# Kernel optimization log

Measured on AMD Instinct MI355X. Metric: run time of the kernel, lower is better.

Reference implementation:

```python
import jax, jax.numpy as jnp
import numpy as np

POOLER_SIZE = 56
SPATIAL_SCALE = 0.25
B, P, K, H, W, A = 4, 512, 4, 200, 336, 14
IMG_H, IMG_W = H / SPATIAL_SCALE, W / SPATIAL_SCALE


def _roi_align_one(feat, boxes):
    """torchvision RoIAlign (aligned=False, sampling_ratio=1).
    feat: [K, H, W]; boxes: [P, 4] as (x1, y1, x2, y2) in image coords.
    Returns [P, K, ps, ps]."""
    Kc, Hf, Wf = feat.shape
    ps = POOLER_SIZE
    s = SPATIAL_SCALE
    x1 = boxes[:, 0] * s
    y1 = boxes[:, 1] * s
    x2 = boxes[:, 2] * s
    y2 = boxes[:, 3] * s
    rw = jnp.maximum(x2 - x1, 1.0)  # non-aligned mode clamps roi size to >= 1
    rh = jnp.maximum(y2 - y1, 1.0)
    bw = rw / ps
    bh = rh / ps
    grid = jnp.arange(ps, dtype=feat.dtype) + 0.5  # sampling_ratio=1 -> bin center
    xs = x1[:, None] + grid[None, :] * bw[:, None]  # [P, ps]
    ys = y1[:, None] + grid[None, :] * bh[:, None]  # [P, ps]
    xx = jnp.broadcast_to(xs[:, None, :], (xs.shape[0], ps, ps))  # [P, ps, ps]
    yy = jnp.broadcast_to(ys[:, :, None], (ys.shape[0], ps, ps))
    valid = (yy > -1.0) & (yy < Hf) & (xx > -1.0) & (xx < Wf)
    y = jnp.clip(yy, 0.0, Hf - 1)
    x = jnp.clip(xx, 0.0, Wf - 1)
    y0 = jnp.floor(y).astype(jnp.int32)
    x0 = jnp.floor(x).astype(jnp.int32)
    y1i = jnp.minimum(y0 + 1, Hf - 1)
    x1i = jnp.minimum(x0 + 1, Wf - 1)
    ly = y - y0
    lx = x - x0
    f = feat.reshape(Kc, Hf * Wf)

    def gather(yi, xi):
        idx = (yi * Wf + xi).reshape(-1)
        return jnp.take(f, idx, axis=1).reshape((Kc,) + yi.shape)  # [K, P, ps, ps]

    w00 = ((1.0 - ly) * (1.0 - lx))[None]
    w01 = ((1.0 - ly) * lx)[None]
    w10 = (ly * (1.0 - lx))[None]
    w11 = (ly * lx)[None]
    v = (gather(y0, x0) * w00 + gather(y0, x1i) * w01 +
         gather(y1i, x0) * w10 + gather(y1i, x1i) * w11)
    v = v * valid[None].astype(feat.dtype)
    return jnp.transpose(v, (1, 0, 2, 3))  # [P, K, ps, ps]


def _bilinear_resize_ac(x, ps):
    """F.interpolate(mode='bilinear', align_corners=True) on last two dims (square a->ps)."""
    a = x.shape[-1]
    src = jnp.arange(ps, dtype=x.dtype) * ((a - 1) / (ps - 1))
    i0 = jnp.clip(jnp.floor(src).astype(jnp.int32), 0, a - 2)
    i1 = i0 + 1
    t = src - i0.astype(x.dtype)
    rows = x[..., i0, :] * (1.0 - t)[:, None] + x[..., i1, :] * t[:, None]  # [..., ps, a]
    out = rows[..., :, i0] * (1.0 - t) + rows[..., :, i1] * t  # [..., ps, ps]
    return out


def setup_inputs() -> dict:
    key = jax.random.key(0)
    k1, k2, k3, k4, k5, k6 = jax.random.split(key, 6)
    bases = jax.random.normal(k1, (B, K, H, W), dtype=jnp.float32)
    attention_proposals = jax.random.normal(k2, (B, P, K, A, A), dtype=jnp.float32)
    # realistic boxes inside an 800x1344 image
    x1 = jax.random.uniform(k3, (B, P)) * (IMG_W - 64.0)
    y1 = jax.random.uniform(k4, (B, P)) * (IMG_H - 64.0)
    bw = 32.0 + jax.random.uniform(k5, (B, P)) * 256.0
    bh = 32.0 + jax.random.uniform(k6, (B, P)) * 256.0
    x2 = jnp.minimum(x1 + bw, IMG_W)
    y2 = jnp.minimum(y1 + bh, IMG_H)
    box_proposals = jnp.stack([x1, y1, x2, y2], axis=-1).astype(jnp.float32)  # [B, P, 4]
    return {"bases": bases, "box_proposals": box_proposals,
            "attention_proposals": attention_proposals}


def reference(bases, box_proposals, attention_proposals):
    ps = POOLER_SIZE
    rois = jax.vmap(_roi_align_one)(bases, box_proposals)  # [B, P, K, ps, ps]
    attn = _bilinear_resize_ac(attention_proposals, ps)    # [B, P, K, ps, ps]
    attn = jax.nn.softmax(attn, axis=2)                    # softmax over num_bases
    return (attn * rois).sum(axis=2)                       # [B, P, ps, ps]
```

## Files before the change

kernel.cpp:

```cpp
#include <hip/hip_runtime.h>
#include <math.h>

#define B_  4
#define P_  512
#define K_  4
#define H_  200
#define W_  336
#define A_  14
#define PS_ 56
#define SCALE_ 0.25f
#define HW_    (H_ * W_)
#define PLB_   (HW_ * 16)
#define ROWB_  (W_ * 16)
#define RROWB_ (PS_ * K_ * 4)

#if __has_builtin(__builtin_amdgcn_exp2f)
#define EXP2F(x) __builtin_amdgcn_exp2f(x)
#else
#define EXP2F(x) exp2f(x)
#endif

static __device__ __forceinline__ unsigned f2bf(float x) {
    unsigned u = __float_as_uint(x);
    return (u + 0x7fffu + ((u >> 16) & 1u)) >> 16;
}
static __device__ __forceinline__ unsigned pk2(float a, float b) {
    return f2bf(a) | (f2bf(b) << 16);
}
#define LOF(u) __uint_as_float((u) << 16)
#define HIF(u) __uint_as_float((u) & 0xffff0000u)

__global__ __launch_bounds__(256) void transpose_bases(
    const float* __restrict__ bases, uint4* __restrict__ ws)
{
    const int i = blockIdx.x * 256 + threadIdx.x;
    if (i >= B_ * HW_) return;
    const int b = i / HW_;
    const int r = i - b * HW_;
    const int x = r % W_;
    const int dn = (x < W_ - 1) ? 1 : 0;
    const float* src = bases + (size_t)b * (K_ * HW_) + r;
    const float v0 = src[0 * HW_],      v1 = src[1 * HW_];
    const float v2 = src[2 * HW_],      v3 = src[3 * HW_];
    const float n0 = src[0 * HW_ + dn], n1 = src[1 * HW_ + dn];
    const float n2 = src[2 * HW_ + dn], n3 = src[3 * HW_ + dn];
    uint4 w;
    w.x = pk2(v0, v1); w.y = pk2(v2, v3);
    w.z = pk2(n0, n1); w.w = pk2(n2, n3);
    ws[i] = w;
}

__global__ __launch_bounds__(448) void blender_kernel(
    const uint4* __restrict__ wsb,
    const float* __restrict__ boxes,
    const float* __restrict__ attn,
    float* __restrict__ out)
{
    const int tid = threadIdx.x;
    const int bp  = blockIdx.x;
    const int b   = bp >> 9;

    __shared__ float  smTile[K_ * A_ * A_];
    __shared__ float  smR[A_ * PS_ * K_];
    __shared__ float4 smX[PS_];
    __shared__ float4 smY[PS_];
    __shared__ float2 smAY[PS_];

    const float* ap = attn + (size_t)bp * (K_ * A_ * A_);
    for (int i = tid; i < K_ * A_ * A_; i += 448)
        smTile[i] = __builtin_nontemporal_load(ap + i);

    const float* bx = boxes + (size_t)bp * 4;
    const float rr = 13.0f / 55.0f;

    if (tid < PS_) {
        const int px = tid;
        const float x1 = bx[0] * SCALE_;
        const float x2 = bx[2] * SCALE_;
        const float bw = fmaxf(x2 - x1, 1.0f) * (1.0f / PS_);
        const float sx = x1 + (px + 0.5f) * bw;
        const float vx = (sx > -1.0f && sx < (float)W_) ? 1.0f : 0.0f;
        const float cx = fminf(fmaxf(sx, 0.0f), (float)(W_ - 1));
        const int   x0 = (int)cx;
        const float lx = cx - (float)x0;
        float4 v;
        v.x = __int_as_float(x0 * 16);
        v.y = (1.0f - lx) * vx;
        v.z = lx * vx;
        v.w = 0.0f;
        smX[px] = v;
    } else if (tid >= 64 && tid < 64 + PS_) {
        const int py = tid - 64;
        const float y1 = bx[1] * SCALE_;
        const float y2 = bx[3] * SCALE_;
        const float bh = fmaxf(y2 - y1, 1.0f) * (1.0f / PS_);
        const float sy = y1 + (py + 0.5f) * bh;
        const float vy = (sy > -1.0f && sy < (float)H_) ? 1.0f : 0.0f;
        const float cy = fminf(fmaxf(sy, 0.0f), (float)(H_ - 1));
        const int   y0 = (int)cy;
        const int   y1i = min(y0 + 1, H_ - 1);
        const float ly = cy - (float)y0;
        float4 v;
        v.x = __int_as_float(y0 * ROWB_);
        v.y = __int_as_float((y1i - y0) * ROWB_);
        v.z = (1.0f - ly) * vy;
        v.w = ly * vy;
        smY[py] = v;
        const float srcy = (float)py * rr;
        const int iy0 = min((int)srcy, A_ - 2);
        float2 a;
        a.x = __int_as_float(iy0 * RROWB_);
        a.y = srcy - (float)iy0;
        smAY[py] = a;
    }
    __syncthreads();

    const float LOG2E = 1.4426950408889634f;
    for (int i = tid; i < K_ * A_ * PS_; i += 448) {
        const int k  = i / (A_ * PS_);
        const int r1 = i - k * (A_ * PS_);
        const int ay = r1 / PS_;
        const int px = r1 - ay * PS_;
        const float srcx = (float)px * rr;
        const int ix0 = min((int)srcx, A_ - 2);
        const float tx = srcx - (float)ix0;
        const float* t = smTile + k * (A_ * A_) + ay * A_ + ix0;
        smR[(ay * PS_ + px) * K_ + k] = (t[0] + tx * (t[1] - t[0])) * LOG2E;
    }
    __syncthreads();

    const char* fb = (const char*)wsb + (size_t)b * PLB_;
    float* outp = out + (size_t)bp * (PS_ * PS_);

    const int px  = tid % PS_;
    const int py0 = tid / PS_;

    const float4 X = smX[px];
    const unsigned xb = (unsigned)__float_as_int(X.x);
    const float wl = X.y, wh = X.z;
    const char* smRbase = (const char*)smR + (px << 4);

    struct PState {
        uint4 r0, r1;
        float wy0, wy1, ty;
        int   ayo;
    };

    auto issue = [&](int t, PState& S) {
        const int py = py0 + 8 * t;
        const float4 Y  = smY[py];
        const float2 AY = smAY[py];
        const unsigned o0 = (unsigned)__float_as_int(Y.x) + xb;
        const unsigned o1 = o0 + (unsigned)__float_as_int(Y.y);
        S.r0 = *(const uint4*)(fb + o0);
        S.r1 = *(const uint4*)(fb + o1);
        S.wy0 = Y.z; S.wy1 = Y.w;
        S.ty = AY.y; S.ayo = __float_as_int(AY.x);
    };

    auto compute = [&](const PState& S) -> float {
        const float wy0 = S.wy0, wy1 = S.wy1, ty = S.ty;
        const float r0a = fmaf(LOF(S.r0.z), wh, LOF(S.r0.x) * wl);
        const float r0b = fmaf(HIF(S.r0.z), wh, HIF(S.r0.x) * wl);
        const float r0c = fmaf(LOF(S.r0.w), wh, LOF(S.r0.y) * wl);
        const float r0d = fmaf(HIF(S.r0.w), wh, HIF(S.r0.y) * wl);
        const float r1a = fmaf(LOF(S.r1.z), wh, LOF(S.r1.x) * wl);
        const float r1b = fmaf(HIF(S.r1.z), wh, HIF(S.r1.x) * wl);
        const float r1c = fmaf(LOF(S.r1.w), wh, LOF(S.r1.y) * wl);
        const float r1d = fmaf(HIF(S.r1.w), wh, HIF(S.r1.y) * wl);
        const float v0 = fmaf(r1a, wy1, r0a * wy0);
        const float v1 = fmaf(r1b, wy1, r0b * wy0);
        const float v2 = fmaf(r1c, wy1, r0c * wy0);
        const float v3 = fmaf(r1d, wy1, r0d * wy0);

        const float4 a0v = *(const float4*)(smRbase + S.ayo);
        const float4 a1v = *(const float4*)(smRbase + S.ayo + RROWB_);
        const float e0 = EXP2F(fmaf(ty, a1v.x - a0v.x, a0v.x));
        const float e1 = EXP2F(fmaf(ty, a1v.y - a0v.y, a0v.y));
        const float e2 = EXP2F(fmaf(ty, a1v.z - a0v.z, a0v.z));
        const float e3 = EXP2F(fmaf(ty, a1v.w - a0v.w, a0v.w));

        const float s = (e0 + e1) + (e2 + e3);
        float acc = e0 * v0;
        acc = fmaf(e1, v1, acc);
        acc = fmaf(e2, v2, acc);
        acc = fmaf(e3, v3, acc);
        return acc * __builtin_amdgcn_rcpf(s);
    };

    PState SA, SB;
    issue(0, SA);
    #pragma unroll
    for (int g = 0; g < 6; g += 2) {
        issue(g + 1, SB);
        __builtin_nontemporal_store(compute(SA), outp + tid + 448 * g);
        issue(g + 2, SA);
        __builtin_nontemporal_store(compute(SB), outp + tid + 448 * (g + 1));
    }
    __builtin_nontemporal_store(compute(SA), outp + tid + 448 * 6);
}

extern "C" void kernel_launch(void* const* d_in, const int* in_sizes, int n_in,
                              void* d_out, int out_size, void* d_ws, size_t ws_size,
                              hipStream_t stream) {
    const float* bases = (const float*)d_in[0];
    const float* boxes = (const float*)d_in[1];
    const float* attn  = (const float*)d_in[2];
    float* out = (float*)d_out;
    uint4* wsb = (uint4*)d_ws;

    transpose_bases<<<dim3((B_ * HW_ + 255) / 256), dim3(256), 0, stream>>>(bases, wsb);
    blender_kernel<<<dim3(B_ * P_), dim3(448), 0, stream>>>(wsb, boxes, attn, out);
}
```

Measured before the change: 90.29 us.

## Halve packed bases workspace and process two ROIs per block

The transpose kernel now packs only the 4 bf16 channels of each pixel into 8 bytes, instead of also storing a copy of the right neighbour. The gather reads 16 unaligned bytes to pick up both the pixel and its right neighbour. This halves workspace writes and the cache footprint. The blender kernel also handles two ROIs per 448-thread block with a reworked pipelined loop, halving block count and spreading setup over more work. Risks: unaligned 16-byte loads may split into two accesses, the final pixel read runs 8 bytes past the workspace end, and fewer blocks may lower occupancy.

```diff
diff --git a/kernel.cpp b/kernel.cpp
--- a/kernel.cpp
+++ b/kernel.cpp
@@ -10,8 +10,8 @@
 #define PS_ 56
 #define SCALE_ 0.25f
 #define HW_    (H_ * W_)
-#define PLB_   (HW_ * 16)
-#define ROWB_  (W_ * 16)
+#define ROWB_  (W_ * 8)
+#define PLB_   (HW_ * 8)
 #define RROWB_ (PS_ * K_ * 4)
 
 #if __has_builtin(__builtin_amdgcn_exp2f)
@@ -30,51 +30,53 @@
 #define LOF(u) __uint_as_float((u) << 16)
 #define HIF(u) __uint_as_float((u) & 0xffff0000u)
 
+static __device__ __forceinline__ uint4 ld16u8(const char* p) {
+    uint4 q;
+    __builtin_memcpy(&q, (const char*)__builtin_assume_aligned(p, 8), 16);
+    return q;
+}
+
 __global__ __launch_bounds__(256) void transpose_bases(
-    const float* __restrict__ bases, uint4* __restrict__ ws)
+    const float* __restrict__ bases, unsigned long long* __restrict__ ws)
 {
     const int i = blockIdx.x * 256 + threadIdx.x;
     if (i >= B_ * HW_) return;
     const int b = i / HW_;
     const int r = i - b * HW_;
-    const int x = r % W_;
-    const int dn = (x < W_ - 1) ? 1 : 0;
     const float* src = bases + (size_t)b * (K_ * HW_) + r;
-    const float v0 = src[0 * HW_],      v1 = src[1 * HW_];
-    const float v2 = src[2 * HW_],      v3 = src[3 * HW_];
-    const float n0 = src[0 * HW_ + dn], n1 = src[1 * HW_ + dn];
-    const float n2 = src[2 * HW_ + dn], n3 = src[3 * HW_ + dn];
-    uint4 w;
-    w.x = pk2(v0, v1); w.y = pk2(v2, v3);
-    w.z = pk2(n0, n1); w.w = pk2(n2, n3);
-    ws[i] = w;
+    const unsigned lo = pk2(src[0 * HW_], src[1 * HW_]);
+    const unsigned hi = pk2(src[2 * HW_], src[3 * HW_]);
+    const unsigned long long w = (unsigned long long)lo
+                               | ((unsigned long long)hi << 32);
+    __builtin_nontemporal_store(w, ws + i);
 }
 
 __global__ __launch_bounds__(448) void blender_kernel(
-    const uint4* __restrict__ wsb,
+    const unsigned long long* __restrict__ wsb,
     const float* __restrict__ boxes,
     const float* __restrict__ attn,
     float* __restrict__ out)
 {
     const int tid = threadIdx.x;
-    const int bp  = blockIdx.x;
-    const int b   = bp >> 9;
-
-    __shared__ float  smTile[K_ * A_ * A_];
-    __shared__ float  smR[A_ * PS_ * K_];
-    __shared__ float4 smX[PS_];
-    __shared__ float4 smY[PS_];
-    __shared__ float2 smAY[PS_];
-
-    const float* ap = attn + (size_t)bp * (K_ * A_ * A_);
-    for (int i = tid; i < K_ * A_ * A_; i += 448)
+    const int bp0 = blockIdx.x * 2;
+    const int b   = bp0 >> 9;
+
+    __shared__ float  smTile[2 * K_ * A_ * A_];
+    __shared__ float  smR[2 * A_ * PS_ * K_];
+    __shared__ float4 smX[2 * PS_];
+    __shared__ float4 smY[2 * PS_];
+    __shared__ float2 smAY[2 * PS_];
+
+    const float* ap = attn + (size_t)bp0 * (K_ * A_ * A_);
+    for (int i = tid; i < 2 * K_ * A_ * A_; i += 448)
         smTile[i] = __builtin_nontemporal_load(ap + i);
 
-    const float* bx = boxes + (size_t)bp * 4;
     const float rr = 13.0f / 55.0f;
 
-    if (tid < PS_) {
-        const int px = tid;
+    if (tid < 112) {
+        const int q  = tid / PS_;
+        const int px = tid - q * PS_;
+        const float* bx = boxes + (size_t)(bp0 + q) * 4;
         const float x1 = bx[0] * SCALE_;
         const float x2 = bx[2] * SCALE_;
         const float bw = fmaxf(x2 - x1, 1.0f) * (1.0f / PS_);
@@ -84,13 +86,16 @@
         const int   x0 = (int)cx;
         const float lx = cx - (float)x0;
         float4 v;
-        v.x = __int_as_float(x0 * 16);
+        v.x = __int_as_float(x0 * 8);
         v.y = (1.0f - lx) * vx;
         v.z = lx * vx;
         v.w = 0.0f;
-        smX[px] = v;
-    } else if (tid >= 64 && tid < 64 + PS_) {
-        const int py = tid - 64;
+        smX[tid] = v;
+    } else if (tid >= 128 && tid < 240) {
+        const int t2 = tid - 128;
+        const int q  = t2 / PS_;
+        const int py = t2 - q * PS_;
+        const float* bx = boxes + (size_t)(bp0 + q) * 4;
         const float y1 = bx[1] * SCALE_;
         const float y2 = bx[3] * SCALE_;
         const float bh = fmaxf(y2 - y1, 1.0f) * (1.0f / PS_);
@@ -105,40 +110,47 @@
         v.y = __int_as_float((y1i - y0) * ROWB_);
         v.z = (1.0f - ly) * vy;
         v.w = ly * vy;
-        smY[py] = v;
+        smY[t2] = v;
         const float srcy = (float)py * rr;
         const int iy0 = min((int)srcy, A_ - 2);
         float2 a;
         a.x = __int_as_float(iy0 * RROWB_);
         a.y = srcy - (float)iy0;
-        smAY[py] = a;
+        smAY[t2] = a;
     }
     __syncthreads();
 
     const float LOG2E = 1.4426950408889634f;
-    for (int i = tid; i < K_ * A_ * PS_; i += 448) {
-        const int k  = i / (A_ * PS_);
-        const int r1 = i - k * (A_ * PS_);
+    for (int i = tid; i < 2 * K_ * A_ * PS_; i += 448) {
+        const int q  = i / (K_ * A_ * PS_);
+        const int j  = i - q * (K_ * A_ * PS_);
+        const int k  = j / (A_ * PS_);
+        const int r1 = j - k * (A_ * PS_);
         const int ay = r1 / PS_;
         const int px = r1 - ay * PS_;
         const float srcx = (float)px * rr;
         const int ix0 = min((int)srcx, A_ - 2);
         const float tx = srcx - (float)ix0;
-        const float* t = smTile + k * (A_ * A_) + ay * A_ + ix0;
-        smR[(ay * PS_ + px) * K_ + k] = (t[0] + tx * (t[1] - t[0])) * LOG2E;
+        const float* t = smTile + q * (K_ * A_ * A_) + k * (A_ * A_) + ay * A_ + ix0;
+        smR[q * (A_ * PS_ * K_) + (ay * PS_ + px) * K_ + k] =
+            (t[0] + tx * (t[1] - t[0])) * LOG2E;
     }
     __syncthreads();
 
     const char* fb = (const char*)wsb + (size_t)b * PLB_;
-    float* outp = out + (size_t)bp * (PS_ * PS_);
-
-    const int px  = tid % PS_;
-    const int py0 = tid / PS_;
-
-    const float4 X = smX[px];
+
+    const int qq  = tid / 224;
+    const int u   = tid - qq * 224;
+    const int px  = u % PS_;
+    const int py0 = u / PS_;
+
+    const float4 X = smX[qq * PS_ + px];
     const unsigned xb = (unsigned)__float_as_int(X.x);
     const float wl = X.y, wh = X.z;
-    const char* smRbase = (const char*)smR + (px << 4);
+    const char* smRbase = (const char*)(smR + qq * (A_ * PS_ * K_)) + (px << 4);
+    float* outq = out + (size_t)(bp0 + qq) * (PS_ * PS_) + py0 * PS_ + px;
+    const float4* smYq  = smY  + qq * PS_;
+    const float2* smAYq = smAY + qq * PS_;
 
     struct PState {
         uint4 r0, r1;
@@ -147,13 +159,13 @@
     };
 
     auto issue = [&](int t, PState& S) {
-        const int py = py0 + 8 * t;
-        const float4 Y  = smY[py];
-        const float2 AY = smAY[py];
+        const int py = py0 + 4 * t;
+        const float4 Y  = smYq[py];
+        const float2 AY = smAYq[py];
         const unsigned o0 = (unsigned)__float_as_int(Y.x) + xb;
         const unsigned o1 = o0 + (unsigned)__float_as_int(Y.y);
-        S.r0 = *(const uint4*)(fb + o0);
-        S.r1 = *(const uint4*)(fb + o1);
+        S.r0 = ld16u8(fb + o0);
+        S.r1 = ld16u8(fb + o1);
         S.wy0 = Y.z; S.wy1 = Y.w;
         S.ty = AY.y; S.ayo = __float_as_int(AY.x);
     };
@@ -190,14 +202,16 @@
 
     PState SA, SB;
     issue(0, SA);
+    issue(1, SB);
     #pragma unroll
-    for (int g = 0; g < 6; g += 2) {
-        issue(g + 1, SB);
-        __builtin_nontemporal_store(compute(SA), outp + tid + 448 * g);
-        issue(g + 2, SA);
-        __builtin_nontemporal_store(compute(SB), outp + tid + 448 * (g + 1));
+    for (int t = 0; t < 12; t += 2) {
+        __builtin_nontemporal_store(compute(SA), outq + t * (4 * PS_));
+        issue(t + 2, SA);
+        __builtin_nontemporal_store(compute(SB), outq + (t + 1) * (4 * PS_));
+        issue(t + 3, SB);
     }
-    __builtin_nontemporal_store(compute(SA), outp + tid + 448 * 6);
+    __builtin_nontemporal_store(compute(SA), outq + 12 * (4 * PS_));
+    __builtin_nontemporal_store(compute(SB), outq + 13 * (4 * PS_));
 }
 
 extern "C" void kernel_launch(void* const* d_in, const int* in_sizes, int n_in,
@@ -207,8 +221,8 @@
     const float* boxes = (const float*)d_in[1];
     const float* attn  = (const float*)d_in[2];
     float* out = (float*)d_out;
-    uint4* wsb = (uint4*)d_ws;
+    unsigned long long* wsb = (unsigned long long*)d_ws;
 
     transpose_bases<<<dim3((B_ * HW_ + 255) / 256), dim3(256), 0, stream>>>(bases, wsb);
-    blender_kernel<<<dim3(B_ * P_), dim3(448), 0, stream>>>(wsb, boxes, attn, out);
-}
+    blender_kernel<<<dim3(B_ * P_ / 2), dim3(448), 0, stream>>>(wsb, boxes, attn, out);
+}
```

Result: no change. 90.79 us (+0.6%).
